# Kernel optimization log

Hardware: AMD Instinct MI355X
Metric: run time of the kernel (lower is better)

The kernel has to match this reference:

```python
import jax, jax.numpy as jnp
import numpy as np

K = 4096          # infeatures
N = 11008         # outfeatures
GROUPSIZE = 128
NG = K // GROUPSIZE  # number of quantization groups
B, S = 2, 2048


def setup_inputs() -> dict:
    key = jax.random.key(0)
    k1, k2, k3, k4, k5 = jax.random.split(key, 5)
    x = jax.random.normal(k1, (B, S, K), dtype=jnp.float32)

    shifts = jnp.arange(8, dtype=jnp.int32) * 4
    # pack 8 int4 nibbles per int32 along the K (row) axis, GPTQ-style
    nib = jax.random.randint(k2, (K, N), 0, 16, dtype=jnp.int32)
    qweight = jnp.sum(nib.reshape(K // 8, 8, N) << shifts[None, :, None], axis=1).astype(jnp.int32)
    # pack 8 int4 zero-points per int32 along the N (col) axis
    znib = jax.random.randint(k3, (NG, N), 0, 16, dtype=jnp.int32)
    qzeros = jnp.sum(znib.reshape(NG, N // 8, 8) << shifts[None, None, :], axis=2).astype(jnp.int32)

    scales = jax.random.uniform(k4, (NG, N), dtype=jnp.float32, minval=1e-3, maxval=1e-2)
    g_idx = (jnp.arange(K) // GROUPSIZE).astype(jnp.int32)
    bias = jax.random.normal(k5, (N,), dtype=jnp.float32) * 0.01
    return {"x": x, "qweight": qweight, "qzeros": qzeros, "scales": scales,
            "g_idx": g_idx, "bias": bias}


def _dequantize(qweight, qzeros, scales, g_idx):
    shifts = jnp.arange(8, dtype=jnp.int32) * 4
    # unpack int4 weights: row r of W comes from qweight[r // 8], nibble r % 8
    q = ((qweight[:, None, :] >> shifts[None, :, None]) & 0xF).reshape(K, N)
    # unpack int4 zero-points (GPTQ stores zero-1, so add 1 back)
    z = (((qzeros[:, :, None] >> shifts[None, None, :]) & 0xF) + 1).reshape(NG, N)
    return (q - z[g_idx]).astype(scales.dtype) * scales[g_idx]  # [K, N]


def reference(x, qweight, qzeros, scales, g_idx, bias):
    W = _dequantize(qweight, qzeros, scales, g_idx)
    return jnp.einsum('bsk,kn->bsn', x, W) + bias
```

## Files before the change

### kernel.cpp

```cpp
#include <hip/hip_runtime.h>

#define M_DIM 4096
#define K_DIM 4096
#define N_DIM 11008
#define GS 128
#define NT 128

typedef _Float16 half8 __attribute__((ext_vector_type(8)));
typedef _Float16 half4 __attribute__((ext_vector_type(4)));
typedef _Float16 half2v __attribute__((ext_vector_type(2)));
typedef float f32x4 __attribute__((ext_vector_type(4)));

#define AH_BYTES 33554432ull
#define WT_BYTES 90177536ull

__global__ __launch_bounds__(256) void cvtA_kernel(const float4* __restrict__ x4,
                                                   half8* __restrict__ a8) {
    int i = blockIdx.x * 256 + threadIdx.x;
    float4 u = x4[2 * i];
    float4 v = x4[2 * i + 1];
    half8 h;
    h[0] = (_Float16)u.x; h[1] = (_Float16)u.y; h[2] = (_Float16)u.z; h[3] = (_Float16)u.w;
    h[4] = (_Float16)v.x; h[5] = (_Float16)v.y; h[6] = (_Float16)v.z; h[7] = (_Float16)v.w;
    a8[i] = h;
}

__global__ __launch_bounds__(256) void dequantW_kernel(const int* __restrict__ qw,
                                                       const int* __restrict__ qz,
                                                       const float* __restrict__ sc,
                                                       _Float16* __restrict__ Wt) {
    const int tk = blockIdx.x & 63;
    const int tn = blockIdx.x >> 6;
    const int k0 = tk * 64, n0 = tn * 64;
    const int g = k0 >> 7;

    __shared__ _Float16 Lt[64][65];

    const int t = threadIdx.x;
    const int n = t & 63;
    const int kwh = t >> 6;
    const int gn = n0 + n;

    float s = sc[(size_t)g * N_DIM + gn];
    int zw = qz[(size_t)g * (N_DIM / 8) + (gn >> 3)];
    int z = ((zw >> ((gn & 7) * 4)) & 0xF) + 1;
    _Float16 sh = (_Float16)s;
    _Float16 zsh = (_Float16)(-(float)z * s);
    half2v s2 = {sh, sh}, zs2 = {zsh, zsh};
    const half2v c1024 = {(_Float16)1024.0f, (_Float16)1024.0f};

    #pragma unroll
    for (int j = 0; j < 2; ++j) {
        int kw = j * 4 + kwh;
        unsigned q = (unsigned)qw[(size_t)(tk * 8 + kw) * N_DIM + gn];
        half2v p[4];
        #pragma unroll
        for (int jj = 0; jj < 4; ++jj) {
            unsigned tt = ((q >> (4 * jj)) & 0x000F000Fu) | 0x64006400u;
            half2v h = __builtin_bit_cast(half2v, tt);
            h = h - c1024;
            p[jj] = h * s2 + zs2;
        }
        int kr = kw * 8;
        Lt[kr + 0][n] = p[0][0]; Lt[kr + 1][n] = p[1][0];
        Lt[kr + 2][n] = p[2][0]; Lt[kr + 3][n] = p[3][0];
        Lt[kr + 4][n] = p[0][1]; Lt[kr + 5][n] = p[1][1];
        Lt[kr + 6][n] = p[2][1]; Lt[kr + 7][n] = p[3][1];
    }
    __syncthreads();

    const int n_l = t >> 2;
    const int c = t & 3;
    half8 o0, o1;
    #pragma unroll
    for (int jj = 0; jj < 8; ++jj) {
        o0[jj] = Lt[c * 16 + jj][n_l];
        o1[jj] = Lt[c * 16 + 8 + jj][n_l];
    }
    size_t base = (size_t)(n0 + n_l) * K_DIM + k0 + c * 16;
    *(half8*)(Wt + base) = o0;
    *(half8*)(Wt + base + 8) = o1;
}


#define SWZ(r) ((((r) >> 1) & 3) << 4)

#define VMC8() asm volatile("s_waitcnt vmcnt(8)" ::: "memory")
#define VMC4() asm volatile("s_waitcnt vmcnt(4)" ::: "memory")
#define VMC0() asm volatile("s_waitcnt vmcnt(0)" ::: "memory")
#define VMCN()

#define STAGE(TILE, UNIT) do {                                                        \
    char* db_ = smem + ((TILE) & 3) * 32768 + ((UNIT) * 16384);                       \
    const char* gb_ = (UNIT) ? wtb : ahb;                                             \
    size_t o0_ = ((UNIT) ? srcB0 : srcA0) + (size_t)(TILE) * 64;                      \
    size_t o1_ = ((UNIT) ? srcB1 : srcA1) + (size_t)(TILE) * 64;                      \
    __builtin_amdgcn_global_load_lds(                                                 \
        (const __attribute__((address_space(1))) void*)(gb_ + o0_),                   \
        (__attribute__((address_space(3))) void*)(db_ + e0 * 1024), 16, 0, 0);        \
    __builtin_amdgcn_global_load_lds(                                                 \
        (const __attribute__((address_space(1))) void*)(gb_ + o1_),                   \
        (__attribute__((address_space(3))) void*)(db_ + e1 * 1024), 16, 0, 0);        \
} while (0)

#define PHASE(CT, MH, STG, VMC) do {                                                  \
    const int cb_ = (CT) & 3;                                                         \
    const char* Ab_ = smem + cb_ * 32768;                                             \
    const char* Bb_ = Ab_ + 16384;                                                    \
    half8 af0 = *(const half8*)(Ab_ + aoff##MH##_0);                                  \
    half8 af1 = *(const half8*)(Ab_ + aoff##MH##_1);                                  \
    half8 af2 = *(const half8*)(Ab_ + aoff##MH##_2);                                  \
    half8 af3 = *(const half8*)(Ab_ + aoff##MH##_3);                                  \
    half8 bf0 = *(const half8*)(Bb_ + boff_0);                                        \
    half8 bf1 = *(const half8*)(Bb_ + boff_1);                                        \
    half8 bf2 = *(const half8*)(Bb_ + boff_2);                                        \
    half8 bf3 = *(const half8*)(Bb_ + boff_3);                                        \
    if (STG) { STAGE((CT) + 3, MH); }                                                 \
    VMC();                                                                            \
    __builtin_amdgcn_s_barrier();                                                     \
    asm volatile("s_waitcnt lgkmcnt(0)" ::: "memory");                                \
    __builtin_amdgcn_sched_barrier(0);                                                \
    __builtin_amdgcn_s_setprio(1);                                                    \
    acc[(MH)*4+0][0] = __builtin_amdgcn_mfma_f32_16x16x32_f16(af0, bf0, acc[(MH)*4+0][0], 0, 0, 0); \
    acc[(MH)*4+0][1] = __builtin_amdgcn_mfma_f32_16x16x32_f16(af0, bf1, acc[(MH)*4+0][1], 0, 0, 0); \
    acc[(MH)*4+0][2] = __builtin_amdgcn_mfma_f32_16x16x32_f16(af0, bf2, acc[(MH)*4+0][2], 0, 0, 0); \
    acc[(MH)*4+0][3] = __builtin_amdgcn_mfma_f32_16x16x32_f16(af0, bf3, acc[(MH)*4+0][3], 0, 0, 0); \
    acc[(MH)*4+1][0] = __builtin_amdgcn_mfma_f32_16x16x32_f16(af1, bf0, acc[(MH)*4+1][0], 0, 0, 0); \
    acc[(MH)*4+1][1] = __builtin_amdgcn_mfma_f32_16x16x32_f16(af1, bf1, acc[(MH)*4+1][1], 0, 0, 0); \
    acc[(MH)*4+1][2] = __builtin_amdgcn_mfma_f32_16x16x32_f16(af1, bf2, acc[(MH)*4+1][2], 0, 0, 0); \
    acc[(MH)*4+1][3] = __builtin_amdgcn_mfma_f32_16x16x32_f16(af1, bf3, acc[(MH)*4+1][3], 0, 0, 0); \
    acc[(MH)*4+2][0] = __builtin_amdgcn_mfma_f32_16x16x32_f16(af2, bf0, acc[(MH)*4+2][0], 0, 0, 0); \
    acc[(MH)*4+2][1] = __builtin_amdgcn_mfma_f32_16x16x32_f16(af2, bf1, acc[(MH)*4+2][1], 0, 0, 0); \
    acc[(MH)*4+2][2] = __builtin_amdgcn_mfma_f32_16x16x32_f16(af2, bf2, acc[(MH)*4+2][2], 0, 0, 0); \
    acc[(MH)*4+2][3] = __builtin_amdgcn_mfma_f32_16x16x32_f16(af2, bf3, acc[(MH)*4+2][3], 0, 0, 0); \
    acc[(MH)*4+3][0] = __builtin_amdgcn_mfma_f32_16x16x32_f16(af3, bf0, acc[(MH)*4+3][0], 0, 0, 0); \
    acc[(MH)*4+3][1] = __builtin_amdgcn_mfma_f32_16x16x32_f16(af3, bf1, acc[(MH)*4+3][1], 0, 0, 0); \
    acc[(MH)*4+3][2] = __builtin_amdgcn_mfma_f32_16x16x32_f16(af3, bf2, acc[(MH)*4+3][2], 0, 0, 0); \
    acc[(MH)*4+3][3] = __builtin_amdgcn_mfma_f32_16x16x32_f16(af3, bf3, acc[(MH)*4+3][3], 0, 0, 0); \
    __builtin_amdgcn_s_setprio(0);                                                    \
    __builtin_amdgcn_s_barrier();                                                     \
} while (0)

__global__ __launch_bounds__(512, 2) void gemm8_kernel(
    const _Float16* __restrict__ Ah,
    const _Float16* __restrict__ Wt,
    const float* __restrict__ bias,
    float* __restrict__ out)
{
    extern __shared__ char smem[];

    const int tid  = threadIdx.x;
    const int lane = tid & 63;
    const int wid  = tid >> 6;
    const int wr   = wid >> 2;
    const int wc   = wid & 3;

    int orig = blockIdx.x;
    int wg = (orig & 7) * 86 + (orig >> 3);
    const int tm = wg / 43;
    const int tn = wg - tm * 43;
    const int m0 = tm * 256;
    const int n0 = tn * 256;

    const char* ahb = (const char*)Ah;
    const char* wtb = (const char*)Wt;

    const int e0 = wid, e1 = wid + 8;
    const int r0 = e0 * 16 + (lane >> 2);
    const int r1 = e1 * 16 + (lane >> 2);
    const int kb0 = ((lane & 3) << 4) ^ SWZ(r0);
    const int kb1 = ((lane & 3) << 4) ^ SWZ(r1);
    const size_t srcA0 = ((size_t)(m0 + r0) << 13) + kb0;
    const size_t srcA1 = ((size_t)(m0 + r1) << 13) + kb1;
    const size_t srcB0 = ((size_t)(n0 + r0) << 13) + kb0;
    const size_t srcB1 = ((size_t)(n0 + r1) << 13) + kb1;

    const int kbr = (lane >> 4) << 4;
    int ra, aoff0_0, aoff0_1, aoff0_2, aoff0_3, aoff1_0, aoff1_1, aoff1_2, aoff1_3;
    ra = wr * 128 +   0 + (lane & 15); aoff0_0 = ra * 64 + (kbr ^ SWZ(ra));
    ra = wr * 128 +  16 + (lane & 15); aoff0_1 = ra * 64 + (kbr ^ SWZ(ra));
    ra = wr * 128 +  32 + (lane & 15); aoff0_2 = ra * 64 + (kbr ^ SWZ(ra));
    ra = wr * 128 +  48 + (lane & 15); aoff0_3 = ra * 64 + (kbr ^ SWZ(ra));
    ra = wr * 128 +  64 + (lane & 15); aoff1_0 = ra * 64 + (kbr ^ SWZ(ra));
    ra = wr * 128 +  80 + (lane & 15); aoff1_1 = ra * 64 + (kbr ^ SWZ(ra));
    ra = wr * 128 +  96 + (lane & 15); aoff1_2 = ra * 64 + (kbr ^ SWZ(ra));
    ra = wr * 128 + 112 + (lane & 15); aoff1_3 = ra * 64 + (kbr ^ SWZ(ra));
    int boff_0, boff_1, boff_2, boff_3;
    ra = wc * 64 +  0 + (lane & 15); boff_0 = ra * 64 + (kbr ^ SWZ(ra));
    ra = wc * 64 + 16 + (lane & 15); boff_1 = ra * 64 + (kbr ^ SWZ(ra));
    ra = wc * 64 + 32 + (lane & 15); boff_2 = ra * 64 + (kbr ^ SWZ(ra));
    ra = wc * 64 + 48 + (lane & 15); boff_3 = ra * 64 + (kbr ^ SWZ(ra));

    f32x4 acc[8][4];
    #pragma unroll
    for (int i = 0; i < 8; ++i)
        #pragma unroll
        for (int j = 0; j < 4; ++j)
            acc[i][j] = f32x4{0.f, 0.f, 0.f, 0.f};

    STAGE(0, 0); STAGE(0, 1);
    STAGE(1, 0); STAGE(1, 1);
    STAGE(2, 0); STAGE(2, 1);
    VMC8();
    __builtin_amdgcn_s_barrier();

    for (int i = 0; i < 31; ++i) {
        const int T = 4 * i;
        PHASE(T + 0, 0, 1, VMCN);
        PHASE(T + 0, 1, 1, VMC8);
        PHASE(T + 1, 0, 1, VMCN);
        PHASE(T + 1, 1, 1, VMC8);
        PHASE(T + 2, 0, 1, VMCN);
        PHASE(T + 2, 1, 1, VMC8);
        PHASE(T + 3, 0, 1, VMCN);
        PHASE(T + 3, 1, 1, VMC8);
    }
    PHASE(124, 0, 1, VMCN);
    PHASE(124, 1, 1, VMC8);
    PHASE(125, 0, 0, VMCN);
    PHASE(125, 1, 0, VMC4);
    PHASE(126, 0, 0, VMCN);
    PHASE(126, 1, 0, VMC0);
    PHASE(127, 0, 0, VMCN);
    PHASE(127, 1, 0, VMCN);

    const int row_base = m0 + wr * 128 + ((lane >> 4) << 2);
    const int col_base = n0 + wc * 64 + (lane & 15);
    #pragma unroll
    for (int ni = 0; ni < 4; ++ni) {
        const int col = col_base + ni * 16;
        const float bv = bias[col];
        #pragma unroll
        for (int mi = 0; mi < 8; ++mi) {
            const int row = row_base + mi * 16;
            #pragma unroll
            for (int j = 0; j < 4; ++j)
                out[(size_t)(row + j) * N_DIM + col] = acc[mi][ni][j] + bv;
        }
    }
}

__global__ __launch_bounds__(256, 2) void gptq_fallback_kernel(
    const float* __restrict__ x, const int* __restrict__ qw, const int* __restrict__ qz,
    const float* __restrict__ sc, const float* __restrict__ bias, float* __restrict__ out)
{
    __shared__ _Float16 As[128 * 64];
    __shared__ _Float16 Bs[128 * 64];
    const int tid = threadIdx.x, lane = tid & 63, wid = tid >> 6;
    const int wr = wid >> 1, wc = wid & 1;
    int orig = blockIdx.x;
    int wg = (orig & 7) * 344 + (orig >> 3);
    const int tm = wg / 86, tn = wg - tm * 86;
    const int m0 = tm * 128, n0 = tn * 128;
    const int a_r0 = tid >> 4, a_c4 = tid & 15;
    const int b_nl = tid & 127, b_qr0 = tid >> 7, b_n = n0 + b_nl;
    const float* xg = x + (size_t)(m0 + a_r0) * K_DIM + a_c4 * 4;
    const int* qwg = qw + (size_t)b_qr0 * N_DIM + b_n;
    float4 areg[8]; int breg[4]; float s_cur, zs_cur;
    #pragma unroll
    for (int i = 0; i < 8; ++i) areg[i] = *(const float4*)(xg + (size_t)i * 16 * K_DIM);
    #pragma unroll
    for (int i = 0; i < 4; ++i) breg[i] = qwg[(size_t)i * 2 * N_DIM];
    { int zw = qz[(size_t)(b_n >> 3)]; int z = ((zw >> ((b_n & 7) * 4)) & 0xF) + 1;
      float s = sc[b_n]; s_cur = s; zs_cur = -(float)z * s; }
    f32x4 acc[4][4];
    #pragma unroll
    for (int i = 0; i < 4; ++i)
        #pragma unroll
        for (int j = 0; j < 4; ++j) acc[i][j] = f32x4{0.f,0.f,0.f,0.f};
    const half2v c1024 = {(_Float16)1024.0f, (_Float16)1024.0f};
    for (int kt = 0; kt < 64; ++kt) {
        if (kt) __syncthreads();
        #pragma unroll
        for (int i = 0; i < 8; ++i) {
            int r = i * 16 + a_r0;
            half4 hv; hv[0]=(_Float16)areg[i].x; hv[1]=(_Float16)areg[i].y;
            hv[2]=(_Float16)areg[i].z; hv[3]=(_Float16)areg[i].w;
            int boff = ((r * 64 + a_c4 * 4) * 2) ^ ((r & 7) << 4);
            *(half4*)((char*)As + boff) = hv;
        }
        { _Float16 sh=(_Float16)s_cur, zsh=(_Float16)zs_cur;
          half2v s2={sh,sh}, zs2={zsh,zsh};
          #pragma unroll
          for (int i = 0; i < 4; ++i) {
            unsigned q = (unsigned)breg[i]; half2v p[4];
            #pragma unroll
            for (int j = 0; j < 4; ++j) {
                unsigned t = ((q >> (4*j)) & 0x000F000Fu) | 0x64006400u;
                half2v h = __builtin_bit_cast(half2v, t); h = h - c1024;
                p[j] = h * s2 + zs2;
            }
            half8 wv; wv[0]=p[0][0]; wv[1]=p[1][0]; wv[2]=p[2][0]; wv[3]=p[3][0];
            wv[4]=p[0][1]; wv[5]=p[1][1]; wv[6]=p[2][1]; wv[7]=p[3][1];
            int qr = b_qr0 + i * 2;
            int boff = ((b_nl * 64 + qr * 8) * 2) ^ ((b_nl & 7) << 4);
            *(half8*)((char*)Bs + boff) = wv;
          } }
        __syncthreads();
        if (kt + 1 < 64) {
            const float* xg2 = xg + (size_t)(kt + 1) * 64;
            #pragma unroll
            for (int i = 0; i < 8; ++i) areg[i] = *(const float4*)(xg2 + (size_t)i * 16 * K_DIM);
            const int* qwg2 = qwg + (size_t)(kt + 1) * 8 * N_DIM;
            #pragma unroll
            for (int i = 0; i < 4; ++i) breg[i] = qwg2[(size_t)i * 2 * N_DIM];
            int g = ((kt + 1) * 64) / GS;
            int zw = qz[(size_t)g * (N_DIM / 8) + (b_n >> 3)];
            int z = ((zw >> ((b_n & 7) * 4)) & 0xF) + 1;
            float s = sc[(size_t)g * N_DIM + b_n];
            s_cur = s; zs_cur = -(float)z * s;
        }
        #pragma unroll
        for (int ks = 0; ks < 2; ++ks) {
            half8 af[4], bf[4];
            int kb = ks * 64 + ((lane >> 4) * 16);
            #pragma unroll
            for (int mi = 0; mi < 4; ++mi) {
                int r = wr * 64 + mi * 16 + (lane & 15);
                int boff = (r * 128 + kb) ^ ((r & 7) << 4);
                af[mi] = *(const half8*)((const char*)As + boff);
            }
            #pragma unroll
            for (int ni = 0; ni < 4; ++ni) {
                int c = wc * 64 + ni * 16 + (lane & 15);
                int boff = (c * 128 + kb) ^ ((c & 7) << 4);
                bf[ni] = *(const half8*)((const char*)Bs + boff);
            }
            #pragma unroll
            for (int mi = 0; mi < 4; ++mi)
                #pragma unroll
                for (int ni = 0; ni < 4; ++ni)
                    acc[mi][ni] = __builtin_amdgcn_mfma_f32_16x16x32_f16(af[mi], bf[ni], acc[mi][ni], 0, 0, 0);
        }
    }
    const int col_base = n0 + wc * 64 + (lane & 15);
    const int row_base = m0 + wr * 64 + ((lane >> 4) << 2);
    #pragma unroll
    for (int ni = 0; ni < 4; ++ni) {
        int col = col_base + ni * 16;
        float bv = bias[col];
        #pragma unroll
        for (int mi = 0; mi < 4; ++mi) {
            int row = row_base + mi * 16;
            #pragma unroll
            for (int j = 0; j < 4; ++j)
                out[(size_t)(row + j) * N_DIM + col] = acc[mi][ni][j] + bv;
        }
    }
}

extern "C" void kernel_launch(void* const* d_in, const int* in_sizes, int n_in,
                              void* d_out, int out_size, void* d_ws, size_t ws_size,
                              hipStream_t stream) {
    const float* x    = (const float*)d_in[0];
    const int*   qw   = (const int*)d_in[1];
    const int*   qz   = (const int*)d_in[2];
    const float* sc   = (const float*)d_in[3];
    const float* bias = (const float*)d_in[5];
    float* out = (float*)d_out;

    if (ws_size >= AH_BYTES + WT_BYTES) {
        _Float16* Ah = (_Float16*)d_ws;
        _Float16* Wt = (_Float16*)((char*)d_ws + AH_BYTES);
        cvtA_kernel<<<8192, 256, 0, stream>>>((const float4*)x, (half8*)Ah);
        dequantW_kernel<<<64 * 172, 256, 0, stream>>>(qw, qz, sc, Wt);
        (void)hipFuncSetAttribute((const void*)gemm8_kernel,
                                  hipFuncAttributeMaxDynamicSharedMemorySize, 131072);
        gemm8_kernel<<<688, 512, 131072, stream>>>(Ah, Wt, bias, out);
    } else {
        gptq_fallback_kernel<<<2752, 256, 0, stream>>>(x, qw, qz, sc, bias, out);
    }
}
```

Before: 632.0 us.

## Shrink GEMM tile to 256x128 with 3-stage pipeline and simpler dequant kernel

The GEMM block tile drops from 256x256 to 256x128, with each of the 8 waves owning a 64x64 sub-tile. The LDS ring changes from 4 stages of 32KB to 3 stages of 24KB, so LDS per block falls from 128KB to 72KB. Launch bounds now target more resident blocks per CU, and the grid doubles to 1376 blocks. The dequant kernel is rewritten to write each thread's 8 K-consecutive halves directly to the transposed layout, removing the LDS transpose and its barrier. The trade-off is lower arithmetic intensity per tile, meaning more global and L2 traffic, and less coalesced dequant stores, in exchange for better occupancy and wave balance.

```diff
diff --git a/kernel.cpp b/kernel.cpp
--- a/kernel.cpp
+++ b/kernel.cpp
@@ -4,7 +4,6 @@
 #define K_DIM 4096
 #define N_DIM 11008
 #define GS 128
-#define NT 128
 
 typedef _Float16 half8 __attribute__((ext_vector_type(8)));
 typedef _Float16 half4 __attribute__((ext_vector_type(4)));
@@ -25,123 +24,99 @@
     a8[i] = h;
 }
 
-__global__ __launch_bounds__(256) void dequantW_kernel(const int* __restrict__ qw,
-                                                       const int* __restrict__ qz,
-                                                       const float* __restrict__ sc,
-                                                       _Float16* __restrict__ Wt) {
-    const int tk = blockIdx.x & 63;
-    const int tn = blockIdx.x >> 6;
-    const int k0 = tk * 64, n0 = tn * 64;
-    const int g = k0 >> 7;
-
-    __shared__ _Float16 Lt[64][65];
-
-    const int t = threadIdx.x;
-    const int n = t & 63;
-    const int kwh = t >> 6;
-    const int gn = n0 + n;
-
-    float s = sc[(size_t)g * N_DIM + gn];
-    int zw = qz[(size_t)g * (N_DIM / 8) + (gn >> 3)];
-    int z = ((zw >> ((gn & 7) * 4)) & 0xF) + 1;
-    _Float16 sh = (_Float16)s;
+__global__ __launch_bounds__(256) void dequantW2_kernel(const int* __restrict__ qw,
+                                                        const int* __restrict__ qz,
+                                                        const float* __restrict__ sc,
+                                                        _Float16* __restrict__ Wt) {
+    const int b   = blockIdx.x;
+    const int nb  = (b % 344) * 32;
+    const int kwb = (b / 344) * 8;
+    const int t   = threadIdx.x;
+    const int l   = t & 63;
+    const int n   = nb + (t >> 6) * 8 + (l >> 3);
+    const int kw  = kwb + (l & 7);
+    const int g   = kwb >> 4;
+
+    float s = sc[(size_t)g * N_DIM + n];
+    int zw = qz[(size_t)g * (N_DIM / 8) + (n >> 3)];
+    int z  = ((zw >> ((n & 7) * 4)) & 0xF) + 1;
+    _Float16 sh  = (_Float16)s;
     _Float16 zsh = (_Float16)(-(float)z * s);
     half2v s2 = {sh, sh}, zs2 = {zsh, zsh};
     const half2v c1024 = {(_Float16)1024.0f, (_Float16)1024.0f};
 
-    #pragma unroll
-    for (int j = 0; j < 2; ++j) {
-        int kw = j * 4 + kwh;
-        unsigned q = (unsigned)qw[(size_t)(tk * 8 + kw) * N_DIM + gn];
-        half2v p[4];
-        #pragma unroll
-        for (int jj = 0; jj < 4; ++jj) {
-            unsigned tt = ((q >> (4 * jj)) & 0x000F000Fu) | 0x64006400u;
-            half2v h = __builtin_bit_cast(half2v, tt);
-            h = h - c1024;
-            p[jj] = h * s2 + zs2;
-        }
-        int kr = kw * 8;
-        Lt[kr + 0][n] = p[0][0]; Lt[kr + 1][n] = p[1][0];
-        Lt[kr + 2][n] = p[2][0]; Lt[kr + 3][n] = p[3][0];
-        Lt[kr + 4][n] = p[0][1]; Lt[kr + 5][n] = p[1][1];
-        Lt[kr + 6][n] = p[2][1]; Lt[kr + 7][n] = p[3][1];
-    }
-    __syncthreads();
-
-    const int n_l = t >> 2;
-    const int c = t & 3;
-    half8 o0, o1;
-    #pragma unroll
-    for (int jj = 0; jj < 8; ++jj) {
-        o0[jj] = Lt[c * 16 + jj][n_l];
-        o1[jj] = Lt[c * 16 + 8 + jj][n_l];
-    }
-    size_t base = (size_t)(n0 + n_l) * K_DIM + k0 + c * 16;
-    *(half8*)(Wt + base) = o0;
-    *(half8*)(Wt + base + 8) = o1;
+    unsigned q = (unsigned)qw[(size_t)kw * N_DIM + n];
+    half2v p[4];
+    #pragma unroll
+    for (int jj = 0; jj < 4; ++jj) {
+        unsigned tt = ((q >> (4 * jj)) & 0x000F000Fu) | 0x64006400u;
+        half2v h = __builtin_bit_cast(half2v, tt);
+        h = h - c1024;
+        p[jj] = h * s2 + zs2;
+    }
+    half8 wv;
+    wv[0] = p[0][0]; wv[1] = p[1][0]; wv[2] = p[2][0]; wv[3] = p[3][0];
+    wv[4] = p[0][1]; wv[5] = p[1][1]; wv[6] = p[2][1]; wv[7] = p[3][1];
+    *(half8*)(Wt + (size_t)n * K_DIM + (size_t)kw * 8) = wv;
 }
 
 
 #define SWZ(r) ((((r) >> 1) & 3) << 4)
 
-#define VMC8() asm volatile("s_waitcnt vmcnt(8)" ::: "memory")
-#define VMC4() asm volatile("s_waitcnt vmcnt(4)" ::: "memory")
+#define VMC3() asm volatile("s_waitcnt vmcnt(3)" ::: "memory")
 #define VMC0() asm volatile("s_waitcnt vmcnt(0)" ::: "memory")
 #define VMCN()
 
-#define STAGE(TILE, UNIT) do {                                                        \
-    char* db_ = smem + ((TILE) & 3) * 32768 + ((UNIT) * 16384);                       \
-    const char* gb_ = (UNIT) ? wtb : ahb;                                             \
-    size_t o0_ = ((UNIT) ? srcB0 : srcA0) + (size_t)(TILE) * 64;                      \
-    size_t o1_ = ((UNIT) ? srcB1 : srcA1) + (size_t)(TILE) * 64;                      \
+#define STAGE3(TT, SB) do {                                                           \
+    char* db_ = smem + (SB) * 24576;                                                  \
     __builtin_amdgcn_global_load_lds(                                                 \
-        (const __attribute__((address_space(1))) void*)(gb_ + o0_),                   \
-        (__attribute__((address_space(3))) void*)(db_ + e0 * 1024), 16, 0, 0);        \
+        (const __attribute__((address_space(1))) void*)(ahb + srcA0 + (size_t)(TT) * 64), \
+        (__attribute__((address_space(3))) void*)(db_ + wid * 1024), 16, 0, 0);       \
     __builtin_amdgcn_global_load_lds(                                                 \
-        (const __attribute__((address_space(1))) void*)(gb_ + o1_),                   \
-        (__attribute__((address_space(3))) void*)(db_ + e1 * 1024), 16, 0, 0);        \
+        (const __attribute__((address_space(1))) void*)(ahb + srcA1 + (size_t)(TT) * 64), \
+        (__attribute__((address_space(3))) void*)(db_ + 8192 + wid * 1024), 16, 0, 0);\
+    __builtin_amdgcn_global_load_lds(                                                 \
+        (const __attribute__((address_space(1))) void*)(wtb + srcB0 + (size_t)(TT) * 64), \
+        (__attribute__((address_space(3))) void*)(db_ + 16384 + wid * 1024), 16, 0, 0);\
 } while (0)
 
-#define PHASE(CT, MH, STG, VMC) do {                                                  \
-    const int cb_ = (CT) & 3;                                                         \
-    const char* Ab_ = smem + cb_ * 32768;                                             \
-    const char* Bb_ = Ab_ + 16384;                                                    \
-    half8 af0 = *(const half8*)(Ab_ + aoff##MH##_0);                                  \
-    half8 af1 = *(const half8*)(Ab_ + aoff##MH##_1);                                  \
-    half8 af2 = *(const half8*)(Ab_ + aoff##MH##_2);                                  \
-    half8 af3 = *(const half8*)(Ab_ + aoff##MH##_3);                                  \
-    half8 bf0 = *(const half8*)(Bb_ + boff_0);                                        \
-    half8 bf1 = *(const half8*)(Bb_ + boff_1);                                        \
-    half8 bf2 = *(const half8*)(Bb_ + boff_2);                                        \
-    half8 bf3 = *(const half8*)(Bb_ + boff_3);                                        \
-    if (STG) { STAGE((CT) + 3, MH); }                                                 \
+#define BODY(CB, SB, STT, STG, VMC) do {                                              \
+    const char* Ab_ = smem + (CB) * 24576;                                            \
+    half8 af0 = *(const half8*)(Ab_ + aoff_0);                                        \
+    half8 af1 = *(const half8*)(Ab_ + aoff_1);                                        \
+    half8 af2 = *(const half8*)(Ab_ + aoff_2);                                        \
+    half8 af3 = *(const half8*)(Ab_ + aoff_3);                                        \
+    half8 bf0 = *(const half8*)(Ab_ + boff_0);                                        \
+    half8 bf1 = *(const half8*)(Ab_ + boff_1);                                        \
+    half8 bf2 = *(const half8*)(Ab_ + boff_2);                                        \
+    half8 bf3 = *(const half8*)(Ab_ + boff_3);                                        \
+    if (STG) { STAGE3((STT), (SB)); }                                                 \
     VMC();                                                                            \
     __builtin_amdgcn_s_barrier();                                                     \
     asm volatile("s_waitcnt lgkmcnt(0)" ::: "memory");                                \
     __builtin_amdgcn_sched_barrier(0);                                                \
     __builtin_amdgcn_s_setprio(1);                                                    \
-    acc[(MH)*4+0][0] = __builtin_amdgcn_mfma_f32_16x16x32_f16(af0, bf0, acc[(MH)*4+0][0], 0, 0, 0); \
-    acc[(MH)*4+0][1] = __builtin_amdgcn_mfma_f32_16x16x32_f16(af0, bf1, acc[(MH)*4+0][1], 0, 0, 0); \
-    acc[(MH)*4+0][2] = __builtin_amdgcn_mfma_f32_16x16x32_f16(af0, bf2, acc[(MH)*4+0][2], 0, 0, 0); \
-    acc[(MH)*4+0][3] = __builtin_amdgcn_mfma_f32_16x16x32_f16(af0, bf3, acc[(MH)*4+0][3], 0, 0, 0); \
-    acc[(MH)*4+1][0] = __builtin_amdgcn_mfma_f32_16x16x32_f16(af1, bf0, acc[(MH)*4+1][0], 0, 0, 0); \
-    acc[(MH)*4+1][1] = __builtin_amdgcn_mfma_f32_16x16x32_f16(af1, bf1, acc[(MH)*4+1][1], 0, 0, 0); \
-    acc[(MH)*4+1][2] = __builtin_amdgcn_mfma_f32_16x16x32_f16(af1, bf2, acc[(MH)*4+1][2], 0, 0, 0); \
-    acc[(MH)*4+1][3] = __builtin_amdgcn_mfma_f32_16x16x32_f16(af1, bf3, acc[(MH)*4+1][3], 0, 0, 0); \
-    acc[(MH)*4+2][0] = __builtin_amdgcn_mfma_f32_16x16x32_f16(af2, bf0, acc[(MH)*4+2][0], 0, 0, 0); \
-    acc[(MH)*4+2][1] = __builtin_amdgcn_mfma_f32_16x16x32_f16(af2, bf1, acc[(MH)*4+2][1], 0, 0, 0); \
-    acc[(MH)*4+2][2] = __builtin_amdgcn_mfma_f32_16x16x32_f16(af2, bf2, acc[(MH)*4+2][2], 0, 0, 0); \
-    acc[(MH)*4+2][3] = __builtin_amdgcn_mfma_f32_16x16x32_f16(af2, bf3, acc[(MH)*4+2][3], 0, 0, 0); \
-    acc[(MH)*4+3][0] = __builtin_amdgcn_mfma_f32_16x16x32_f16(af3, bf0, acc[(MH)*4+3][0], 0, 0, 0); \
-    acc[(MH)*4+3][1] = __builtin_amdgcn_mfma_f32_16x16x32_f16(af3, bf1, acc[(MH)*4+3][1], 0, 0, 0); \
-    acc[(MH)*4+3][2] = __builtin_amdgcn_mfma_f32_16x16x32_f16(af3, bf2, acc[(MH)*4+3][2], 0, 0, 0); \
-    acc[(MH)*4+3][3] = __builtin_amdgcn_mfma_f32_16x16x32_f16(af3, bf3, acc[(MH)*4+3][3], 0, 0, 0); \
+    acc[0][0] = __builtin_amdgcn_mfma_f32_16x16x32_f16(af0, bf0, acc[0][0], 0, 0, 0); \
+    acc[0][1] = __builtin_amdgcn_mfma_f32_16x16x32_f16(af0, bf1, acc[0][1], 0, 0, 0); \
+    acc[0][2] = __builtin_amdgcn_mfma_f32_16x16x32_f16(af0, bf2, acc[0][2], 0, 0, 0); \
+    acc[0][3] = __builtin_amdgcn_mfma_f32_16x16x32_f16(af0, bf3, acc[0][3], 0, 0, 0); \
+    acc[1][0] = __builtin_amdgcn_mfma_f32_16x16x32_f16(af1, bf0, acc[1][0], 0, 0, 0); \
+    acc[1][1] = __builtin_amdgcn_mfma_f32_16x16x32_f16(af1, bf1, acc[1][1], 0, 0, 0); \
+    acc[1][2] = __builtin_amdgcn_mfma_f32_16x16x32_f16(af1, bf2, acc[1][2], 0, 0, 0); \
+    acc[1][3] = __builtin_amdgcn_mfma_f32_16x16x32_f16(af1, bf3, acc[1][3], 0, 0, 0); \
+    acc[2][0] = __builtin_amdgcn_mfma_f32_16x16x32_f16(af2, bf0, acc[2][0], 0, 0, 0); \
+    acc[2][1] = __builtin_amdgcn_mfma_f32_16x16x32_f16(af2, bf1, acc[2][1], 0, 0, 0); \
+    acc[2][2] = __builtin_amdgcn_mfma_f32_16x16x32_f16(af2, bf2, acc[2][2], 0, 0, 0); \
+    acc[2][3] = __builtin_amdgcn_mfma_f32_16x16x32_f16(af2, bf3, acc[2][3], 0, 0, 0); \
+    acc[3][0] = __builtin_amdgcn_mfma_f32_16x16x32_f16(af3, bf0, acc[3][0], 0, 0, 0); \
+    acc[3][1] = __builtin_amdgcn_mfma_f32_16x16x32_f16(af3, bf1, acc[3][1], 0, 0, 0); \
+    acc[3][2] = __builtin_amdgcn_mfma_f32_16x16x32_f16(af3, bf2, acc[3][2], 0, 0, 0); \
+    acc[3][3] = __builtin_amdgcn_mfma_f32_16x16x32_f16(af3, bf3, acc[3][3], 0, 0, 0); \
     __builtin_amdgcn_s_setprio(0);                                                    \
     __builtin_amdgcn_s_barrier();                                                     \
 } while (0)
 
-__global__ __launch_bounds__(512, 2) void gemm8_kernel(
+__global__ __launch_bounds__(512, 4) void gemm9_kernel(
     const _Float16* __restrict__ Ah,
     const _Float16* __restrict__ Wt,
     const float* __restrict__ bias,
@@ -152,86 +127,65 @@
     const int tid  = threadIdx.x;
     const int lane = tid & 63;
     const int wid  = tid >> 6;
-    const int wr   = wid >> 2;
-    const int wc   = wid & 3;
+    const int wr   = wid >> 1;
+    const int wc   = wid & 1;
 
     int orig = blockIdx.x;
-    int wg = (orig & 7) * 86 + (orig >> 3);
-    const int tm = wg / 43;
-    const int tn = wg - tm * 43;
+    int wg = (orig & 7) * 172 + (orig >> 3);
+    const int tm = wg / 86;
+    const int tn = wg - tm * 86;
     const int m0 = tm * 256;
-    const int n0 = tn * 256;
+    const int n0 = tn * 128;
 
     const char* ahb = (const char*)Ah;
     const char* wtb = (const char*)Wt;
 
-    const int e0 = wid, e1 = wid + 8;
-    const int r0 = e0 * 16 + (lane >> 2);
-    const int r1 = e1 * 16 + (lane >> 2);
-    const int kb0 = ((lane & 3) << 4) ^ SWZ(r0);
-    const int kb1 = ((lane & 3) << 4) ^ SWZ(r1);
-    const size_t srcA0 = ((size_t)(m0 + r0) << 13) + kb0;
-    const size_t srcA1 = ((size_t)(m0 + r1) << 13) + kb1;
-    const size_t srcB0 = ((size_t)(n0 + r0) << 13) + kb0;
-    const size_t srcB1 = ((size_t)(n0 + r1) << 13) + kb1;
-
-    const int kbr = (lane >> 4) << 4;
-    int ra, aoff0_0, aoff0_1, aoff0_2, aoff0_3, aoff1_0, aoff1_1, aoff1_2, aoff1_3;
-    ra = wr * 128 +   0 + (lane & 15); aoff0_0 = ra * 64 + (kbr ^ SWZ(ra));
-    ra = wr * 128 +  16 + (lane & 15); aoff0_1 = ra * 64 + (kbr ^ SWZ(ra));
-    ra = wr * 128 +  32 + (lane & 15); aoff0_2 = ra * 64 + (kbr ^ SWZ(ra));
-    ra = wr * 128 +  48 + (lane & 15); aoff0_3 = ra * 64 + (kbr ^ SWZ(ra));
-    ra = wr * 128 +  64 + (lane & 15); aoff1_0 = ra * 64 + (kbr ^ SWZ(ra));
-    ra = wr * 128 +  80 + (lane & 15); aoff1_1 = ra * 64 + (kbr ^ SWZ(ra));
-    ra = wr * 128 +  96 + (lane & 15); aoff1_2 = ra * 64 + (kbr ^ SWZ(ra));
-    ra = wr * 128 + 112 + (lane & 15); aoff1_3 = ra * 64 + (kbr ^ SWZ(ra));
-    int boff_0, boff_1, boff_2, boff_3;
-    ra = wc * 64 +  0 + (lane & 15); boff_0 = ra * 64 + (kbr ^ SWZ(ra));
-    ra = wc * 64 + 16 + (lane & 15); boff_1 = ra * 64 + (kbr ^ SWZ(ra));
-    ra = wc * 64 + 32 + (lane & 15); boff_2 = ra * 64 + (kbr ^ SWZ(ra));
-    ra = wc * 64 + 48 + (lane & 15); boff_3 = ra * 64 + (kbr ^ SWZ(ra));
-
-    f32x4 acc[8][4];
-    #pragma unroll
-    for (int i = 0; i < 8; ++i)
+    const int rS  = wid * 16 + (lane >> 2);
+    const int kbS = ((lane & 3) << 4) ^ SWZ(rS);
+    const size_t srcA0 = ((size_t)(m0 + rS) << 13) + kbS;
+    const size_t srcA1 = ((size_t)(m0 + rS + 128) << 13) + kbS;
+    const size_t srcB0 = ((size_t)(n0 + rS) << 13) + kbS;
+
+    const int klane = (lane >> 4) << 4;
+    int ra, aoff_0, aoff_1, aoff_2, aoff_3, boff_0, boff_1, boff_2, boff_3;
+    ra = wr * 64 +  0 + (lane & 15); aoff_0 = ra * 64 + (klane ^ SWZ(ra));
+    ra = wr * 64 + 16 + (lane & 15); aoff_1 = ra * 64 + (klane ^ SWZ(ra));
+    ra = wr * 64 + 32 + (lane & 15); aoff_2 = ra * 64 + (klane ^ SWZ(ra));
+    ra = wr * 64 + 48 + (lane & 15); aoff_3 = ra * 64 + (klane ^ SWZ(ra));
+    ra = wc * 64 +  0 + (lane & 15); boff_0 = 16384 + ra * 64 + (klane ^ SWZ(ra));
+    ra = wc * 64 + 16 + (lane & 15); boff_1 = 16384 + ra * 64 + (klane ^ SWZ(ra));
+    ra = wc * 64 + 32 + (lane & 15); boff_2 = 16384 + ra * 64 + (klane ^ SWZ(ra));
+    ra = wc * 64 + 48 + (lane & 15); boff_3 = 16384 + ra * 64 + (klane ^ SWZ(ra));
+
+    f32x4 acc[4][4];
+    #pragma unroll
+    for (int i = 0; i < 4; ++i)
         #pragma unroll
         for (int j = 0; j < 4; ++j)
             acc[i][j] = f32x4{0.f, 0.f, 0.f, 0.f};
 
-    STAGE(0, 0); STAGE(0, 1);
-    STAGE(1, 0); STAGE(1, 1);
-    STAGE(2, 0); STAGE(2, 1);
-    VMC8();
+    STAGE3(0, 0);
+    STAGE3(1, 1);
+    VMC3();
     __builtin_amdgcn_s_barrier();
 
-    for (int i = 0; i < 31; ++i) {
-        const int T = 4 * i;
-        PHASE(T + 0, 0, 1, VMCN);
-        PHASE(T + 0, 1, 1, VMC8);
-        PHASE(T + 1, 0, 1, VMCN);
-        PHASE(T + 1, 1, 1, VMC8);
-        PHASE(T + 2, 0, 1, VMCN);
-        PHASE(T + 2, 1, 1, VMC8);
-        PHASE(T + 3, 0, 1, VMCN);
-        PHASE(T + 3, 1, 1, VMC8);
-    }
-    PHASE(124, 0, 1, VMCN);
-    PHASE(124, 1, 1, VMC8);
-    PHASE(125, 0, 0, VMCN);
-    PHASE(125, 1, 0, VMC4);
-    PHASE(126, 0, 0, VMCN);
-    PHASE(126, 1, 0, VMC0);
-    PHASE(127, 0, 0, VMCN);
-    PHASE(127, 1, 0, VMCN);
-
-    const int row_base = m0 + wr * 128 + ((lane >> 4) << 2);
+    for (int it = 0; it < 42; ++it) {
+        const int T = 3 * it;
+        BODY(0, 2, T + 2, 1, VMC3);
+        BODY(1, 0, T + 3, 1, VMC3);
+        BODY(2, 1, T + 4, 1, VMC3);
+    }
+    BODY(0, 2, 0, 0, VMC0);
+    BODY(1, 0, 0, 0, VMCN);
+
+    const int row_base = m0 + wr * 64 + ((lane >> 4) << 2);
     const int col_base = n0 + wc * 64 + (lane & 15);
     #pragma unroll
     for (int ni = 0; ni < 4; ++ni) {
         const int col = col_base + ni * 16;
         const float bv = bias[col];
         #pragma unroll
-        for (int mi = 0; mi < 8; ++mi) {
+        for (int mi = 0; mi < 4; ++mi) {
             const int row = row_base + mi * 16;
             #pragma unroll
             for (int j = 0; j < 4; ++j)
@@ -363,10 +317,10 @@
         _Float16* Ah = (_Float16*)d_ws;
         _Float16* Wt = (_Float16*)((char*)d_ws + AH_BYTES);
         cvtA_kernel<<<8192, 256, 0, stream>>>((const float4*)x, (half8*)Ah);
-        dequantW_kernel<<<64 * 172, 256, 0, stream>>>(qw, qz, sc, Wt);
-        (void)hipFuncSetAttribute((const void*)gemm8_kernel,
-                                  hipFuncAttributeMaxDynamicSharedMemorySize, 131072);
-        gemm8_kernel<<<688, 512, 131072, stream>>>(Ah, Wt, bias, out);
+        dequantW2_kernel<<<344 * 64, 256, 0, stream>>>(qw, qz, sc, Wt);
+        (void)hipFuncSetAttribute((const void*)gemm9_kernel,
+                                  hipFuncAttributeMaxDynamicSharedMemorySize, 73728);
+        gemm9_kernel<<<1376, 512, 73728, stream>>>(Ah, Wt, bias, out);
     } else {
         gptq_fallback_kernel<<<2752, 256, 0, stream>>>(x, qw, qz, sc, bias, out);
     }
```

New measurement: 633.4 us. Within noise of the previous version (+0.2%).
